# Kernel tuning notes

Hardware: AMD Instinct MI355X
Metric: run time of the kernel (lower is better)

The kernel has to match this reference:

```python
import jax, jax.numpy as jnp
import numpy as np
from jax import lax

EPS = 1e-3  # keras LayerNormalization default epsilon


def _conv(x, w, padding):
    return lax.conv_general_dilated(x, w, (1, 1), padding,
                                    dimension_numbers=('NHWC', 'HWIO', 'NHWC'))


def _hard_sigmoid(x):
    return jnp.clip(0.2 * x + 0.5, 0.0, 1.0)


def _layernorm(x, g, b):
    mu = jnp.mean(x, axis=-1, keepdims=True)
    var = jnp.mean(jnp.square(x - mu), axis=-1, keepdims=True)
    return (x - mu) * lax.rsqrt(var + EPS) * g + b


def _convlstm(x, W, U, b, return_sequences):
    # x: [B,T,H,Wd,C]; W: [5,5,C,4F] (valid); U: [5,5,F,4F] (same); b: [4F]
    B, T, H, Wd, C = x.shape
    F = U.shape[2]
    xg = _conv(x.reshape(B * T, H, Wd, C), W, 'VALID') + b
    Ho, Wo = xg.shape[1], xg.shape[2]
    xg = xg.reshape(B, T, Ho, Wo, 4 * F).transpose(1, 0, 2, 3, 4)  # time-major

    def step(carry, xt):
        h, c = carry
        g = xt + _conv(h, U, 'SAME')
        i, f, cg, o = jnp.split(g, 4, axis=-1)
        i = _hard_sigmoid(i)
        f = _hard_sigmoid(f)
        o = _hard_sigmoid(o)
        c = f * c + i * jnp.tanh(cg)
        h = o * jnp.tanh(c)
        return (h, c), h

    h0 = jnp.zeros((B, Ho, Wo, F), x.dtype)
    (h, c), hs = lax.scan(step, (h0, h0), xg)
    return hs.transpose(1, 0, 2, 3, 4) if return_sequences else h


def setup_inputs() -> dict:
    key = jax.random.key(0)
    ks = jax.random.split(key, 8)
    B, T, H, Wd, C = 8, 16, 40, 40, 16
    F = 64
    s = lambda *sh: 1.0 / np.sqrt(np.prod(sh[:-1]))
    x = jax.random.normal(ks[0], (B, T, H, Wd, C), jnp.float32)
    W1 = jax.random.normal(ks[1], (5, 5, C, 4 * F), jnp.float32) * s(5, 5, C, 1)
    U1 = jax.random.normal(ks[2], (5, 5, F, 4 * F), jnp.float32) * s(5, 5, F, 1)
    W2 = jax.random.normal(ks[3], (5, 5, F, 4 * F), jnp.float32) * s(5, 5, F, 1)
    U2 = jax.random.normal(ks[4], (5, 5, F, 4 * F), jnp.float32) * s(5, 5, F, 1)
    return {
        'x': x,
        'ln_g1': jnp.ones((C,), jnp.float32), 'ln_b1': jnp.zeros((C,), jnp.float32),
        'W1': W1, 'U1': U1, 'b1': jnp.zeros((4 * F,), jnp.float32),
        'ln_g2': jnp.ones((F,), jnp.float32), 'ln_b2': jnp.zeros((F,), jnp.float32),
        'W2': W2, 'U2': U2, 'b2': jnp.zeros((4 * F,), jnp.float32),
        'dw': jax.random.normal(ks[5], (F, 1), jnp.float32) * (1.0 / np.sqrt(F)),
        'db': jnp.zeros((1,), jnp.float32),
    }


OUTPUT_SCALE = 0.1


def reference(x, ln_g1, ln_b1, W1, U1, b1, ln_g2, ln_b2, W2, U2, b2, dw, db):
    h = _layernorm(x, ln_g1, ln_b1)
    h = _convlstm(h, W1, U1, b1, return_sequences=True)   # [B,T,36,36,F]
    h = _layernorm(h, ln_g2, ln_b2)
    h = _convlstm(h, W2, U2, b2, return_sequences=False)  # [B,32,32,F]
    pooled = jnp.mean(h, axis=(1, 2))                     # [B,F]
    y = pooled @ dw + db                                  # [B,1]
    return y.reshape(-1) * OUTPUT_SCALE
```

## Files before the change

kernel.cpp:

```cpp
#include <hip/hip_runtime.h>
#include <hip/hip_bf16.h>
#include <cstddef>

#define LN_EPS 1e-3f

typedef short bf16x8 __attribute__((ext_vector_type(8)));
typedef float f32x4 __attribute__((ext_vector_type(4)));

__device__ __forceinline__ unsigned short f2bf(float f) {
    __hip_bfloat16 b = __float2bfloat16(f);
    unsigned short u;
    __builtin_memcpy(&u, &b, 2);
    return u;
}

__device__ __forceinline__ float hsig(float x) {
    return fminf(fmaxf(fmaf(x, 0.2f, 0.5f), 0.f), 1.f);
}

__global__ void ln16_kernel(const float* __restrict__ x, const float* __restrict__ g,
                            const float* __restrict__ b, float* __restrict__ y, int rows)
{
    int r = blockIdx.x * 256 + threadIdx.x;
    if (r >= rows) return;
    const float4* xr = (const float4*)(x + (size_t)r * 16);
    float v[16];
    *(float4*)(v + 0)  = xr[0];
    *(float4*)(v + 4)  = xr[1];
    *(float4*)(v + 8)  = xr[2];
    *(float4*)(v + 12) = xr[3];
    float mu = 0.f;
    #pragma unroll
    for (int i = 0; i < 16; ++i) mu += v[i];
    mu *= (1.f / 16.f);
    float var = 0.f;
    #pragma unroll
    for (int i = 0; i < 16; ++i) { float d = v[i] - mu; var += d * d; }
    var *= (1.f / 16.f);
    float rs = rsqrtf(var + LN_EPS);
    float o[16];
    #pragma unroll
    for (int i = 0; i < 16; ++i) o[i] = (v[i] - mu) * rs * g[i] + b[i];
    float4* yr = (float4*)(y + (size_t)r * 16);
    yr[0] = *(float4*)(o + 0);
    yr[1] = *(float4*)(o + 4);
    yr[2] = *(float4*)(o + 8);
    yr[3] = *(float4*)(o + 12);
}

__global__ void ln64_kernel(const float* __restrict__ x, const float* __restrict__ g,
                            const float* __restrict__ b, float* __restrict__ y, int rows)
{
    int gidx = blockIdx.x * 256 + threadIdx.x;
    int row  = gidx >> 6;
    int lane = gidx & 63;
    if (row >= rows) return;
    float v = x[(size_t)row * 64 + lane];
    float s = v;
    #pragma unroll
    for (int o = 32; o > 0; o >>= 1) s += __shfl_xor(s, o);
    float mu = s * (1.f / 64.f);
    float d = v - mu;
    float q = d * d;
    #pragma unroll
    for (int o = 32; o > 0; o >>= 1) q += __shfl_xor(q, o);
    float rs = rsqrtf(q * (1.f / 64.f) + LN_EPS);
    y[(size_t)row * 64 + lane] = d * rs * g[lane] + b[lane];
}

__global__ void prep_w_perm(const float* __restrict__ w, short* __restrict__ o, int K, int NC)
{
    int e = blockIdx.x * 256 + threadIdx.x;
    int tot = NC * 32 * 256;
    if (e >= tot) return;
    int cop = e & 255;
    int k   = e >> 8;
    int qq   = cop >> 6;
    int wn   = (cop >> 5) & 1;
    int gate = (cop >> 3) & 3;
    int fl   = cop & 7;
    int fg = qq * 16 + wn * 8 + fl;
    int co_orig = gate * 64 + fg;
    float v = (k < K) ? w[(size_t)k * 256 + co_orig] : 0.f;
    int chunk = k >> 5, kk = k & 31;
    o[((size_t)chunk * 256 + cop) * 32 + kk] = (short)f2bf(v);
}

template<int CIN, int PAD, int PRN, int PW, bool ZEROROW>
__device__ __forceinline__ void stage_patch(char* smem, const float* __restrict__ inN,
                                            int IH, int IW, int r0)
{
    constexpr int GPP = CIN / 8;
    constexpr int SH  = (CIN == 64) ? 7 : 6;
    constexpr int TOTG = PRN * PW * GPP;
    const int tid = threadIdx.x;
    for (int gg = tid; gg < TOTG; gg += 256) {
        int pix = gg / GPP;
        int cig = gg % GPP;
        int pr = pix / PW, pc = pix % PW;
        int gy = r0 - PAD + pr;
        int gx = pc - PAD;
        float v[8] = {0.f,0.f,0.f,0.f,0.f,0.f,0.f,0.f};
        bool ok = (gy >= 0) & (gy < IH) & (gx >= 0) & (gx < IW);
        if (ZEROROW && pr == PRN - 1) ok = false;
        if (ok) {
            const float* p = inN + ((size_t)gy * IW + gx) * CIN + cig * 8;
            float4 f0 = *(const float4*)p;
            float4 f1 = *(const float4*)(p + 4);
            v[0]=f0.x; v[1]=f0.y; v[2]=f0.z; v[3]=f0.w;
            v[4]=f1.x; v[5]=f1.y; v[6]=f1.z; v[7]=f1.w;
        }
        union { bf16x8 v8; unsigned short u[8]; } pk;
        #pragma unroll
        for (int i = 0; i < 8; ++i) pk.u[i] = f2bf(v[i]);
        int ad = (pix * CIN + cig * 8) * 2;
        ad ^= ((ad >> SH) & 7) << 4;
        *(bf16x8*)(smem + ad) = pk.v8;
    }
}

template<int CIN, int PW, int NC>
__device__ __forceinline__ void kloop(const char* smem, const short* __restrict__ wbase,
                                      int colane, int g, const int* base_m, f32x4 (&acc)[4][2])
{
    constexpr int SH = (CIN == 64) ? 7 : 6;
    const short* wlp = wbase + (size_t)colane * 32 + g * 8;
    bf16x8 bc0 = *(const bf16x8*)wlp;
    bf16x8 bc1 = *(const bf16x8*)(wlp + 512);
    int dy0 = 0, dx0 = 0, dy1 = 0, dx1 = 1;
    for (int c = 0; c < NC; ++c) {
        bf16x8 bn0, bn1;
        const bool pf = (c + 1 < NC);
        if (pf) {
            const short* wnx = wlp + (size_t)(c + 1) * 8192;
            bn0 = *(const bf16x8*)wnx;
            bn1 = *(const bf16x8*)(wnx + 512);
        }
        int off;
        if (CIN == 64) {
            off = (dy0 * PW + dx0) * 128 + ((c & 1) << 6) + (g << 4);
        } else {
            int U0 = (dy0 * PW + dx0) * 32;
            int U1 = (dy1 * PW + dx1) * 32;
            off = ((g & 2) ? U1 : U0) + ((g & 1) << 4);
        }
        bf16x8 a[4];
        #pragma unroll
        for (int m = 0; m < 4; ++m) {
            int ad = base_m[m] + off;
            ad ^= ((ad >> SH) & 7) << 4;
            a[m] = *(const bf16x8*)(smem + ad);
        }
        #pragma unroll
        for (int m = 0; m < 4; ++m) {
            acc[m][0] = __builtin_amdgcn_mfma_f32_16x16x32_bf16(a[m], bc0, acc[m][0], 0, 0, 0);
            acc[m][1] = __builtin_amdgcn_mfma_f32_16x16x32_bf16(a[m], bc1, acc[m][1], 0, 0, 0);
        }
        if (pf) { bc0 = bn0; bc1 = bn1; }
        if (CIN == 64) {
            if (c & 1) { if (++dx0 == 5) { dx0 = 0; ++dy0; } }
        } else {
            dx0 += 2; if (dx0 >= 5) { dx0 -= 5; ++dy0; }
            dx1 += 2; if (dx1 >= 5) { dx1 -= 5; ++dy1; }
        }
    }
}

template<int CIN1, int PAD1, int NC1, int PRN1, bool ZR1,
         int NC2, int PRN2, int OW, int OH>
__device__ void lstm_step_core(int lblk, const float* __restrict__ in1, size_t in1_bstride,
                               int IH1, int IW1,
                               const float* __restrict__ hprev,
                               const short* __restrict__ wts, const float* __restrict__ bias,
                               float* __restrict__ cbuf, float* __restrict__ hbuf,
                               int has_rec, char* smem)
{
    constexpr int PW  = OW + 4;
    constexpr int OHW = OW * OH;
    constexpr int NTIL = (OHW + 127) / 128;
    constexpr bool FULL = (OHW % 128) == 0;

    const int tid  = threadIdx.x;
    const int tile = lblk % NTIL;
    const int q    = (lblk / NTIL) & 3;
    const int n    = lblk / (NTIL * 4);
    const int p0   = tile * 128;
    const int r0   = p0 / OW;
    const int co0  = q * 64;

    const int lane = tid & 63;
    const int wid  = tid >> 6;
    const int wm   = wid >> 1;
    const int wn   = wid & 1;
    const int lr   = lane & 15;
    const int g    = lane >> 4;

    int base1[4], base2[4];
    #pragma unroll
    for (int m = 0; m < 4; ++m) {
        int px = p0 + wm * 64 + m * 16 + lr;
        int r = px / OW;
        int x = px - r * OW;
        base1[m] = ((r - r0) * PW + x) * CIN1 * 2;
        base2[m] = ((r - r0) * PW + x) * 128;
    }

    f32x4 acc[4][2];
    #pragma unroll
    for (int m = 0; m < 4; ++m)
        #pragma unroll
        for (int nn = 0; nn < 2; ++nn)
            acc[m][nn] = (f32x4){0.f, 0.f, 0.f, 0.f};

    stage_patch<CIN1, PAD1, PRN1, PW, ZR1>(smem, in1 + (size_t)n * in1_bstride, IH1, IW1, r0);
    __syncthreads();
    kloop<CIN1, PW, NC1>(smem, wts, co0 + wn * 32 + lr, g, base1, acc);

    if (has_rec) {
        __syncthreads();
        stage_patch<64, 2, PRN2, PW, false>(smem, hprev + (size_t)n * OHW * 64, OH, OW, r0);
        __syncthreads();
        kloop<64, PW, NC2>(smem, wts + (size_t)NC1 * 8192, co0 + wn * 32 + lr, g, base2, acc);
    }

    const int fg = q * 16 + wn * 8 + (lr & 7);
    const bool low = (lr & 8) == 0;
    const float b0  = bias[(lr >> 3) * 64 + fg];
    const float b1v = bias[(2 + (lr >> 3)) * 64 + fg];
    float* cN = cbuf + (size_t)n * OHW * 64;
    float* hN = hbuf + (size_t)n * OHW * 64;
    #pragma unroll
    for (int m = 0; m < 4; ++m) {
        int pxb = p0 + wm * 64 + m * 16 + g * 4;
        #pragma unroll
        for (int j = 0; j < 4; ++j) {
            int px = pxb + j;
            float a0 = acc[m][0][j] + b0;
            float a1 = acc[m][1][j] + b1v;
            float q0 = __shfl_xor(a0, 8);
            float q1 = __shfl_xor(a1, 8);
            float iv  = low ? a0 : q0;
            float fv  = low ? q0 : a0;
            float cgv = low ? a1 : q1;
            float ov  = low ? q1 : a1;
            bool valid = FULL || (px < OHW);
            int addr = px * 64 + fg;
            float cp = 0.f;
            if (has_rec && valid) cp = cN[addr];
            float cn = fmaf(hsig(fv), cp, hsig(iv) * tanhf(cgv));
            float hv = hsig(ov) * tanhf(cn);
            if (valid) {
                if (low) cN[addr] = cn;
                else     hN[addr] = hv;
            }
        }
    }
}

__global__ __launch_bounds__(256, 3) void step_kernel(
    int n2, int has1, int has2,
    const float* __restrict__ hln,  const float* __restrict__ h2r, float* __restrict__ h2w,
    float* __restrict__ c2, const short* __restrict__ w2c, const float* __restrict__ b2,
    const float* __restrict__ xlnt, const float* __restrict__ h1r, float* __restrict__ h1w,
    float* __restrict__ c1, const short* __restrict__ w1c, const float* __restrict__ b1)
{
    __shared__ __align__(16) char smem[46080];
    int bid = blockIdx.x;
    if (bid < n2) {
        lstm_step_core<64, 0, 50, 8, false, 50, 8, 32, 32>(
            bid, hln, 82944, 36, 36, h2r, w2c, b2, c2, h2w, has2, smem);
    } else {
        lstm_step_core<16, 0, 13, 10, true, 50, 9, 36, 36>(
            bid - n2, xlnt, 409600, 40, 40, h1r, w1c, b1, c1, h1w, has1, smem);
    }
}

__global__ void pool_dot_kernel(const float* __restrict__ h, const float* __restrict__ dw,
                                const float* __restrict__ db, float* __restrict__ out)
{
    int b = blockIdx.x;
    __shared__ float sdw[64];
    if (threadIdx.x < 64) sdw[threadIdx.x] = dw[threadIdx.x];
    __syncthreads();
    float partial = 0.f;
    const float* hb = h + (size_t)b * 1024 * 64;
    for (int p = threadIdx.x; p < 1024; p += 256) {
        const float* hp = hb + (size_t)p * 64;
        #pragma unroll
        for (int f = 0; f < 64; f += 4) {
            float4 hv = *(const float4*)(hp + f);
            partial += hv.x * sdw[f] + hv.y * sdw[f + 1] + hv.z * sdw[f + 2] + hv.w * sdw[f + 3];
        }
    }
    #pragma unroll
    for (int o = 32; o > 0; o >>= 1) partial += __shfl_xor(partial, o);
    __shared__ float ws[4];
    if ((threadIdx.x & 63) == 0) ws[threadIdx.x >> 6] = partial;
    __syncthreads();
    if (threadIdx.x == 0) {
        float tot = ws[0] + ws[1] + ws[2] + ws[3];
        out[b] = (tot * (1.f / 1024.f) + db[0]) * 0.1f;
    }
}

extern "C" void kernel_launch(void* const* d_in, const int* in_sizes, int n_in,
                              void* d_out, int out_size, void* d_ws, size_t ws_size,
                              hipStream_t stream)
{
    const float* x   = (const float*)d_in[0];
    const float* lg1 = (const float*)d_in[1];
    const float* lb1 = (const float*)d_in[2];
    const float* W1  = (const float*)d_in[3];
    const float* U1  = (const float*)d_in[4];
    const float* b1  = (const float*)d_in[5];
    const float* lg2 = (const float*)d_in[6];
    const float* lb2 = (const float*)d_in[7];
    const float* W2  = (const float*)d_in[8];
    const float* U2  = (const float*)d_in[9];
    const float* b2  = (const float*)d_in[10];
    const float* dw  = (const float*)d_in[11];
    const float* db  = (const float*)d_in[12];
    float* out = (float*)d_out;

    constexpr int B = 8, T = 16;
    constexpr int P1 = 36 * 36, P2 = 32 * 32;

    float* w = (float*)d_ws;
    size_t off = 0;
    float* xln = w + off; off += (size_t)B * T * 40 * 40 * 16;
    float* h1a = w + off; off += (size_t)B * P1 * 64;
    float* h1b = w + off; off += (size_t)B * P1 * 64;
    float* c1  = w + off; off += (size_t)B * P1 * 64;
    float* hln = w + off; off += (size_t)B * P1 * 64;
    float* h2a = w + off; off += (size_t)B * P2 * 64;
    float* h2b = w + off; off += (size_t)B * P2 * 64;
    float* c2  = w + off; off += (size_t)B * P2 * 64;
    short* w1c = (short*)(w + off); off += (size_t)63 * 8192 / 2;
    short* w2c = (short*)(w + off); off += (size_t)100 * 8192 / 2;

    float* h1buf[2] = { h1a, h1b };
    float* h2buf[2] = { h2a, h2b };

    ln16_kernel<<<800, 256, 0, stream>>>(x, lg1, lb1, xln, 204800);
    prep_w_perm<<<416, 256, 0, stream>>>(W1, w1c, 400, 13);
    prep_w_perm<<<1600, 256, 0, stream>>>(U1, w1c + (size_t)13 * 8192, 1600, 50);
    prep_w_perm<<<1600, 256, 0, stream>>>(W2, w2c, 1600, 50);
    prep_w_perm<<<1600, 256, 0, stream>>>(U2, w2c + (size_t)50 * 8192, 1600, 50);

    constexpr int NB1 = 11 * 4 * B;
    constexpr int NB2 = 8 * 4 * B;

    step_kernel<<<NB1, 256, 0, stream>>>(
        0, 0, 0,
        hln, h2buf[1], h2buf[0], c2, w2c, b2,
        xln, h1buf[1], h1buf[0], c1, w1c, b1);
    ln64_kernel<<<2592, 256, 0, stream>>>(h1buf[0], lg2, lb2, hln, B * P1);

    for (int t = 0; t < T - 1; ++t) {
        step_kernel<<<NB2 + NB1, 256, 0, stream>>>(
            NB2, 1, (t > 0) ? 1 : 0,
            hln, h2buf[(t + 1) & 1], h2buf[t & 1], c2, w2c, b2,
            xln + (size_t)(t + 1) * 25600, h1buf[t & 1], h1buf[(t + 1) & 1], c1, w1c, b1);
        ln64_kernel<<<2592, 256, 0, stream>>>(h1buf[(t + 1) & 1], lg2, lb2, hln, B * P1);
    }

    step_kernel<<<NB2, 256, 0, stream>>>(
        NB2, 1, 1,
        hln, h2buf[0], h2buf[1], c2, w2c, b2,
        xln, h1buf[1], h1buf[0], c1, w1c, b1);

    pool_dot_kernel<<<B, 256, 0, stream>>>(h2buf[1], dw, db, out);
}
```

Measured before the change: 956.7 us.

## Fuse layer-2 LayerNorm into patch staging and store activations in bf16

Removes the separate ln64 kernel launch that ran every timestep and instead applies the LayerNorm inside the layer-2 patch staging, using an 8-lane shuffle reduction over each pixel's 64 channels. Hidden states and the layer-1 normalised input are now stored in bf16, which halves global traffic and drops the per-stage float-to-bf16 conversion. The weight prefetch in the MFMA k-loop also moves from one chunk ahead to two. The LayerNorm is now recomputed for halo pixels in every tile, and its statistics come from already bf16-rounded h values, which adds a small precision difference.

```diff
diff --git a/kernel.cpp b/kernel.cpp
--- a/kernel.cpp
+++ b/kernel.cpp
@@ -14,12 +14,19 @@
     return u;
 }
 
+__device__ __forceinline__ float bf2f(short u) {
+    unsigned int x = ((unsigned int)(unsigned short)u) << 16;
+    float f;
+    __builtin_memcpy(&f, &x, 4);
+    return f;
+}
+
 __device__ __forceinline__ float hsig(float x) {
     return fminf(fmaxf(fmaf(x, 0.2f, 0.5f), 0.f), 1.f);
 }
 
 __global__ void ln16_kernel(const float* __restrict__ x, const float* __restrict__ g,
-                            const float* __restrict__ b, float* __restrict__ y, int rows)
+                            const float* __restrict__ b, short* __restrict__ y, int rows)
 {
     int r = blockIdx.x * 256 + threadIdx.x;
     if (r >= rows) return;
@@ -38,34 +45,14 @@
     for (int i = 0; i < 16; ++i) { float d = v[i] - mu; var += d * d; }
     var *= (1.f / 16.f);
     float rs = rsqrtf(var + LN_EPS);
-    float o[16];
-    #pragma unroll
-    for (int i = 0; i < 16; ++i) o[i] = (v[i] - mu) * rs * g[i] + b[i];
-    float4* yr = (float4*)(y + (size_t)r * 16);
-    yr[0] = *(float4*)(o + 0);
-    yr[1] = *(float4*)(o + 4);
-    yr[2] = *(float4*)(o + 8);
-    yr[3] = *(float4*)(o + 12);
-}
-
-__global__ void ln64_kernel(const float* __restrict__ x, const float* __restrict__ g,
-                            const float* __restrict__ b, float* __restrict__ y, int rows)
-{
-    int gidx = blockIdx.x * 256 + threadIdx.x;
-    int row  = gidx >> 6;
-    int lane = gidx & 63;
-    if (row >= rows) return;
-    float v = x[(size_t)row * 64 + lane];
-    float s = v;
-    #pragma unroll
-    for (int o = 32; o > 0; o >>= 1) s += __shfl_xor(s, o);
-    float mu = s * (1.f / 64.f);
-    float d = v - mu;
-    float q = d * d;
-    #pragma unroll
-    for (int o = 32; o > 0; o >>= 1) q += __shfl_xor(q, o);
-    float rs = rsqrtf(q * (1.f / 64.f) + LN_EPS);
-    y[(size_t)row * 64 + lane] = d * rs * g[lane] + b[lane];
+    union { bf16x8 v8; unsigned short u[8]; } p0, p1;
+    #pragma unroll
+    for (int i = 0; i < 8; ++i)  p0.u[i] = f2bf((v[i] - mu) * rs * g[i] + b[i]);
+    #pragma unroll
+    for (int i = 0; i < 8; ++i)  p1.u[i] = f2bf((v[8 + i] - mu) * rs * g[8 + i] + b[8 + i]);
+    bf16x8* yr = (bf16x8*)(y + (size_t)r * 16);
+    yr[0] = p0.v8;
+    yr[1] = p1.v8;
 }
 
 __global__ void prep_w_perm(const float* __restrict__ w, short* __restrict__ o, int K, int NC)
@@ -86,9 +73,11 @@
     o[((size_t)chunk * 256 + cop) * 32 + kk] = (short)f2bf(v);
 }
 
-template<int CIN, int PAD, int PRN, int PW, bool ZEROROW>
-__device__ __forceinline__ void stage_patch(char* smem, const float* __restrict__ inN,
-                                            int IH, int IW, int r0)
+template<int CIN, int PAD, int PRN, int PW, bool ZEROROW, bool DOLN>
+__device__ __forceinline__ void stage_patch(char* smem, const short* __restrict__ inN,
+                                            int IH, int IW, int r0,
+                                            const float* __restrict__ lg,
+                                            const float* __restrict__ lb)
 {
     constexpr int GPP = CIN / 8;
     constexpr int SH  = (CIN == 64) ? 7 : 6;
@@ -100,22 +89,37 @@
         int pr = pix / PW, pc = pix % PW;
         int gy = r0 - PAD + pr;
         int gx = pc - PAD;
-        float v[8] = {0.f,0.f,0.f,0.f,0.f,0.f,0.f,0.f};
         bool ok = (gy >= 0) & (gy < IH) & (gx >= 0) & (gx < IW);
         if (ZEROROW && pr == PRN - 1) ok = false;
-        if (ok) {
-            const float* p = inN + ((size_t)gy * IW + gx) * CIN + cig * 8;
-            float4 f0 = *(const float4*)p;
-            float4 f1 = *(const float4*)(p + 4);
-            v[0]=f0.x; v[1]=f0.y; v[2]=f0.z; v[3]=f0.w;
-            v[4]=f1.x; v[5]=f1.y; v[6]=f1.z; v[7]=f1.w;
-        }
-        union { bf16x8 v8; unsigned short u[8]; } pk;
-        #pragma unroll
-        for (int i = 0; i < 8; ++i) pk.u[i] = f2bf(v[i]);
+        bf16x8 v;
+        #pragma unroll
+        for (int i = 0; i < 8; ++i) v[i] = 0;
+        if (ok) v = *(const bf16x8*)(inN + ((size_t)gy * IW + gx) * CIN + cig * 8);
+        if (DOLN) {
+            float f[8];
+            #pragma unroll
+            for (int i = 0; i < 8; ++i) f[i] = bf2f(v[i]);
+            float s = 0.f;
+            #pragma unroll
+            for (int i = 0; i < 8; ++i) s += f[i];
+            s += __shfl_xor(s, 1); s += __shfl_xor(s, 2); s += __shfl_xor(s, 4);
+            float mu = s * (1.f / 64.f);
+            float q = 0.f;
+            #pragma unroll
+            for (int i = 0; i < 8; ++i) { float d = f[i] - mu; q += d * d; }
+            q += __shfl_xor(q, 1); q += __shfl_xor(q, 2); q += __shfl_xor(q, 4);
+            float rs = rsqrtf(q * (1.f / 64.f) + LN_EPS);
+            union { bf16x8 v8; unsigned short u[8]; } pk;
+            #pragma unroll
+            for (int i = 0; i < 8; ++i) {
+                int ch = cig * 8 + i;
+                pk.u[i] = f2bf((f[i] - mu) * rs * lg[ch] + lb[ch]);
+            }
+            v = pk.v8;
+        }
         int ad = (pix * CIN + cig * 8) * 2;
         ad ^= ((ad >> SH) & 7) << 4;
-        *(bf16x8*)(smem + ad) = pk.v8;
+        *(bf16x8*)(smem + ad) = v;
     }
 }
 
@@ -125,16 +129,21 @@
 {
     constexpr int SH = (CIN == 64) ? 7 : 6;
     const short* wlp = wbase + (size_t)colane * 32 + g * 8;
-    bf16x8 bc0 = *(const bf16x8*)wlp;
-    bf16x8 bc1 = *(const bf16x8*)(wlp + 512);
+    bf16x8 c0a = *(const bf16x8*)wlp;
+    bf16x8 c0b = *(const bf16x8*)(wlp + 512);
+    bf16x8 c1a, c1b;
+    if (NC > 1) {
+        c1a = *(const bf16x8*)(wlp + 8192);
+        c1b = *(const bf16x8*)(wlp + 8192 + 512);
+    }
     int dy0 = 0, dx0 = 0, dy1 = 0, dx1 = 1;
     for (int c = 0; c < NC; ++c) {
-        bf16x8 bn0, bn1;
-        const bool pf = (c + 1 < NC);
+        bf16x8 n2a, n2b;
+        const bool pf = (c + 2 < NC);
         if (pf) {
-            const short* wnx = wlp + (size_t)(c + 1) * 8192;
-            bn0 = *(const bf16x8*)wnx;
-            bn1 = *(const bf16x8*)(wnx + 512);
+            const short* wnx = wlp + (size_t)(c + 2) * 8192;
+            n2a = *(const bf16x8*)wnx;
+            n2b = *(const bf16x8*)(wnx + 512);
         }
         int off;
         if (CIN == 64) {
@@ -153,10 +162,11 @@
         }
         #pragma unroll
         for (int m = 0; m < 4; ++m) {
-            acc[m][0] = __builtin_amdgcn_mfma_f32_16x16x32_bf16(a[m], bc0, acc[m][0], 0, 0, 0);
-            acc[m][1] = __builtin_amdgcn_mfma_f32_16x16x32_bf16(a[m], bc1, acc[m][1], 0, 0, 0);
-        }
-        if (pf) { bc0 = bn0; bc1 = bn1; }
+            acc[m][0] = __builtin_amdgcn_mfma_f32_16x16x32_bf16(a[m], c0a, acc[m][0], 0, 0, 0);
+            acc[m][1] = __builtin_amdgcn_mfma_f32_16x16x32_bf16(a[m], c0b, acc[m][1], 0, 0, 0);
+        }
+        c0a = c1a; c0b = c1b;
+        if (pf) { c1a = n2a; c1b = n2b; }
         if (CIN == 64) {
             if (c & 1) { if (++dx0 == 5) { dx0 = 0; ++dy0; } }
         } else {
@@ -166,13 +176,14 @@
     }
 }
 
-template<int CIN1, int PAD1, int NC1, int PRN1, bool ZR1,
+template<int CIN1, int PAD1, int NC1, int PRN1, bool ZR1, bool DOLN1,
          int NC2, int PRN2, int OW, int OH>
-__device__ void lstm_step_core(int lblk, const float* __restrict__ in1, size_t in1_bstride,
+__device__ void lstm_step_core(int lblk, const short* __restrict__ in1, size_t in1_bstride,
                                int IH1, int IW1,
-                               const float* __restrict__ hprev,
+                               const short* __restrict__ hprev,
                                const short* __restrict__ wts, const float* __restrict__ bias,
-                               float* __restrict__ cbuf, float* __restrict__ hbuf,
+                               const float* __restrict__ lg, const float* __restrict__ lb,
+                               float* __restrict__ cbuf, short* __restrict__ hbuf,
                                int has_rec, char* smem)
 {
     constexpr int PW  = OW + 4;
@@ -212,13 +223,15 @@
         for (int nn = 0; nn < 2; ++nn)
             acc[m][nn] = (f32x4){0.f, 0.f, 0.f, 0.f};
 
-    stage_patch<CIN1, PAD1, PRN1, PW, ZR1>(smem, in1 + (size_t)n * in1_bstride, IH1, IW1, r0);
+    stage_patch<CIN1, PAD1, PRN1, PW, ZR1, DOLN1>(
+        smem, in1 + (size_t)n * in1_bstride, IH1, IW1, r0, lg, lb);
     __syncthreads();
     kloop<CIN1, PW, NC1>(smem, wts, co0 + wn * 32 + lr, g, base1, acc);
 
     if (has_rec) {
         __syncthreads();
-        stage_patch<64, 2, PRN2, PW, false>(smem, hprev + (size_t)n * OHW * 64, OH, OW, r0);
+        stage_patch<64, 2, PRN2, PW, false, false>(
+            smem, hprev + (size_t)n * OHW * 64, OH, OW, r0, nullptr, nullptr);
         __syncthreads();
         kloop<64, PW, NC2>(smem, wts + (size_t)NC1 * 8192, co0 + wn * 32 + lr, g, base2, acc);
     }
@@ -228,7 +241,7 @@
     const float b0  = bias[(lr >> 3) * 64 + fg];
     const float b1v = bias[(2 + (lr >> 3)) * 64 + fg];
     float* cN = cbuf + (size_t)n * OHW * 64;
-    float* hN = hbuf + (size_t)n * OHW * 64;
+    short* hN = hbuf + (size_t)n * OHW * 64;
     #pragma unroll
     for (int m = 0; m < 4; ++m) {
         int pxb = p0 + wm * 64 + m * 16 + g * 4;
@@ -251,7 +264,7 @@
             float hv = hsig(ov) * tanhf(cn);
             if (valid) {
                 if (low) cN[addr] = cn;
-                else     hN[addr] = hv;
+                else     hN[addr] = (short)f2bf(hv);
             }
         }
     }
@@ -259,23 +272,25 @@
 
 __global__ __launch_bounds__(256, 3) void step_kernel(
     int n2, int has1, int has2,
-    const float* __restrict__ hln,  const float* __restrict__ h2r, float* __restrict__ h2w,
+    const short* __restrict__ h1r, const short* __restrict__ h2r, short* __restrict__ h2w,
     float* __restrict__ c2, const short* __restrict__ w2c, const float* __restrict__ b2,
-    const float* __restrict__ xlnt, const float* __restrict__ h1r, float* __restrict__ h1w,
+    const float* __restrict__ lg2, const float* __restrict__ lb2,
+    const short* __restrict__ xlnt, short* __restrict__ h1w,
     float* __restrict__ c1, const short* __restrict__ w1c, const float* __restrict__ b1)
 {
     __shared__ __align__(16) char smem[46080];
     int bid = blockIdx.x;
     if (bid < n2) {
-        lstm_step_core<64, 0, 50, 8, false, 50, 8, 32, 32>(
-            bid, hln, 82944, 36, 36, h2r, w2c, b2, c2, h2w, has2, smem);
+        lstm_step_core<64, 0, 50, 8, false, true, 50, 8, 32, 32>(
+            bid, h1r, 82944, 36, 36, h2r, w2c, b2, lg2, lb2, c2, h2w, has2, smem);
     } else {
-        lstm_step_core<16, 0, 13, 10, true, 50, 9, 36, 36>(
-            bid - n2, xlnt, 409600, 40, 40, h1r, w1c, b1, c1, h1w, has1, smem);
-    }
-}
-
-__global__ void pool_dot_kernel(const float* __restrict__ h, const float* __restrict__ dw,
+        lstm_step_core<16, 0, 13, 10, true, false, 50, 9, 36, 36>(
+            bid - n2, xlnt, 409600, 40, 40, h1r, w1c, b1, nullptr, nullptr,
+            c1, h1w, has1, smem);
+    }
+}
+
+__global__ void pool_dot_kernel(const short* __restrict__ h, const float* __restrict__ dw,
                                 const float* __restrict__ db, float* __restrict__ out)
 {
     int b = blockIdx.x;
@@ -283,13 +298,14 @@
     if (threadIdx.x < 64) sdw[threadIdx.x] = dw[threadIdx.x];
     __syncthreads();
     float partial = 0.f;
-    const float* hb = h + (size_t)b * 1024 * 64;
+    const short* hb = h + (size_t)b * 1024 * 64;
     for (int p = threadIdx.x; p < 1024; p += 256) {
-        const float* hp = hb + (size_t)p * 64;
-        #pragma unroll
-        for (int f = 0; f < 64; f += 4) {
-            float4 hv = *(const float4*)(hp + f);
-            partial += hv.x * sdw[f] + hv.y * sdw[f + 1] + hv.z * sdw[f + 2] + hv.w * sdw[f + 3];
+        const short* hp = hb + (size_t)p * 64;
+        #pragma unroll
+        for (int f = 0; f < 64; f += 8) {
+            bf16x8 hv = *(const bf16x8*)(hp + f);
+            #pragma unroll
+            for (int i = 0; i < 8; ++i) partial += bf2f(hv[i]) * sdw[f + i];
         }
     }
     #pragma unroll
@@ -325,21 +341,23 @@
     constexpr int B = 8, T = 16;
     constexpr int P1 = 36 * 36, P2 = 32 * 32;
 
-    float* w = (float*)d_ws;
+    char* wsb = (char*)d_ws;
     size_t off = 0;
-    float* xln = w + off; off += (size_t)B * T * 40 * 40 * 16;
-    float* h1a = w + off; off += (size_t)B * P1 * 64;
-    float* h1b = w + off; off += (size_t)B * P1 * 64;
-    float* c1  = w + off; off += (size_t)B * P1 * 64;
-    float* hln = w + off; off += (size_t)B * P1 * 64;
-    float* h2a = w + off; off += (size_t)B * P2 * 64;
-    float* h2b = w + off; off += (size_t)B * P2 * 64;
-    float* c2  = w + off; off += (size_t)B * P2 * 64;
-    short* w1c = (short*)(w + off); off += (size_t)63 * 8192 / 2;
-    short* w2c = (short*)(w + off); off += (size_t)100 * 8192 / 2;
-
-    float* h1buf[2] = { h1a, h1b };
-    float* h2buf[2] = { h2a, h2b };
+    auto alloc_s = [&](size_t nshort) { short* p = (short*)(wsb + off); off += nshort * 2; return p; };
+    auto alloc_f = [&](size_t nfloat) { off = (off + 15) & ~(size_t)15; float* p = (float*)(wsb + off); off += nfloat * 4; return p; };
+
+    short* xln = alloc_s((size_t)B * T * 40 * 40 * 16);
+    short* h1a = alloc_s((size_t)B * P1 * 64);
+    short* h1b = alloc_s((size_t)B * P1 * 64);
+    short* h2a = alloc_s((size_t)B * P2 * 64);
+    short* h2b = alloc_s((size_t)B * P2 * 64);
+    short* w1c = alloc_s((size_t)63 * 8192);
+    short* w2c = alloc_s((size_t)100 * 8192);
+    float* c1  = alloc_f((size_t)B * P1 * 64);
+    float* c2  = alloc_f((size_t)B * P2 * 64);
+
+    short* h1buf[2] = { h1a, h1b };
+    short* h2buf[2] = { h2a, h2b };
 
     ln16_kernel<<<800, 256, 0, stream>>>(x, lg1, lb1, xln, 204800);
     prep_w_perm<<<416, 256, 0, stream>>>(W1, w1c, 400, 13);
@@ -352,22 +370,20 @@
 
     step_kernel<<<NB1, 256, 0, stream>>>(
         0, 0, 0,
-        hln, h2buf[1], h2buf[0], c2, w2c, b2,
-        xln, h1buf[1], h1buf[0], c1, w1c, b1);
-    ln64_kernel<<<2592, 256, 0, stream>>>(h1buf[0], lg2, lb2, hln, B * P1);
+        h1buf[1], h2buf[1], h2buf[0], c2, w2c, b2, lg2, lb2,
+        xln, h1buf[0], c1, w1c, b1);
 
     for (int t = 0; t < T - 1; ++t) {
         step_kernel<<<NB2 + NB1, 256, 0, stream>>>(
             NB2, 1, (t > 0) ? 1 : 0,
-            hln, h2buf[(t + 1) & 1], h2buf[t & 1], c2, w2c, b2,
-            xln + (size_t)(t + 1) * 25600, h1buf[t & 1], h1buf[(t + 1) & 1], c1, w1c, b1);
-        ln64_kernel<<<2592, 256, 0, stream>>>(h1buf[(t + 1) & 1], lg2, lb2, hln, B * P1);
+            h1buf[t & 1], h2buf[(t + 1) & 1], h2buf[t & 1], c2, w2c, b2, lg2, lb2,
+            xln + (size_t)(t + 1) * 25600, h1buf[(t + 1) & 1], c1, w1c, b1);
     }
 
     step_kernel<<<NB2, 256, 0, stream>>>(
         NB2, 1, 1,
-        hln, h2buf[0], h2buf[1], c2, w2c, b2,
-        xln, h1buf[1], h1buf[0], c1, w1c, b1);
+        h1buf[1], h2buf[0], h2buf[1], c2, w2c, b2, lg2, lb2,
+        xln, h1buf[0], c1, w1c, b1);
 
     pool_dot_kernel<<<B, 256, 0, stream>>>(h2buf[1], dw, db, out);
 }
```

New measurement: 871.1 us. 9.0% less time.
